# Performance work log

Measured on AMD Instinct MI355X. Metric: run time of the kernel, lower is better.

Reference implementation:

```python
import jax, jax.numpy as jnp
from jax import lax
import numpy as np

N_FFT = 256
HOP = 128
NUM_EXPERTS = 8
TOPK = 2
B = 128
L = 4096


def conv1d(x, w, b, pad):
    # x [N,C,T], w [O,I,K]
    y = lax.conv_general_dilated(x, w, (1,), [(pad, pad)],
                                 dimension_numbers=('NCH', 'OIH', 'NCH'))
    return y + b[None, :, None]


def maxpool1d(x, p):
    return lax.reduce_window(x, -jnp.inf, lax.max, (1, 1, p), (1, 1, p), 'VALID')


def se_block(x, w1, w2):
    # x [B,C,T]; squeeze-excitation with no-bias linears
    y = x.mean(-1)
    y = jax.nn.relu(y @ w1.T)
    y = jax.nn.sigmoid(y @ w2.T)
    return x * y[:, :, None]


def interp_linear(x, out_len):
    # F.interpolate(mode='linear', align_corners=False) on [B,C,T]
    Lin = x.shape[-1]
    scale = Lin / out_len
    coords = jnp.clip((jnp.arange(out_len, dtype=x.dtype) + 0.5) * scale - 0.5, 0.0, Lin - 1)
    lo = jnp.floor(coords).astype(jnp.int32)
    hi = jnp.minimum(lo + 1, Lin - 1)
    w = (coords - lo).astype(x.dtype)
    return x[..., lo] * (1.0 - w) + x[..., hi] * w


def lstm_scan(x, wih, whh, bih, bhh):
    # x [T,B,D] -> hidden seq [T,B,H]; torch gate order i,f,g,o
    H = whh.shape[1]
    def step(carry, xt):
        h, c = carry
        gates = xt @ wih.T + h @ whh.T + bih + bhh
        i, f, g, o = jnp.split(gates, 4, axis=-1)
        c = jax.nn.sigmoid(f) * c + jax.nn.sigmoid(i) * jnp.tanh(g)
        h = jax.nn.sigmoid(o) * jnp.tanh(c)
        return (h, c), h
    z = jnp.zeros((x.shape[1], H), x.dtype)
    _, hs = lax.scan(step, (z, z), x)
    return hs


def _forward(x_continuum, x_normalized,
             gate_w1, gate_b1, gate_w2, gate_b2,
             exp_w1, exp_b1, exp_w2, exp_b2,
             lw1, lb1, lw2, lb2, se2_w1, se2_w2, lw3, lb3, se3_w1, se3_w2,
             wih_f, whh_f, bih_f, bhh_f, wih_b, whh_b, bih_b, bhh_b,
             ffn_w1, ffn_b1, ffn_w2, ffn_b2):
    Bsz = x_continuum.shape[0]
    # --- STFT magnitude (center=True, reflect pad, periodic hann window) ---
    n = jnp.arange(N_FFT, dtype=x_continuum.dtype)
    win = 0.5 * (1.0 - jnp.cos(2.0 * jnp.pi * n / N_FFT))
    xp = jnp.pad(x_continuum, ((0, 0), (N_FFT // 2, N_FFT // 2)), mode='reflect')
    n_frames = 1 + (xp.shape[1] - N_FFT) // HOP  # 33
    idx = jnp.arange(n_frames)[:, None] * HOP + jnp.arange(N_FFT)[None, :]
    frames = xp[:, idx] * win                      # [B,T,N_FFT]
    mag = jnp.abs(jnp.fft.rfft(frames, axis=-1)).transpose(0, 2, 1)  # [B,129,T]
    mag = mag.astype(x_continuum.dtype)
    # --- gating: mean-pool over time, MLP, top-k, softmax over top-k ---
    pooled = mag.mean(-1)                          # [B,129]
    logits = jax.nn.relu(pooled @ gate_w1.T + gate_b1) @ gate_w2.T + gate_b2
    topv, topi = lax.top_k(logits, TOPK)
    gw = jax.nn.softmax(topv, axis=1)              # [B,K]
    # --- dense all-expert conv pyramids (matches original dense compute) ---
    def expert(w1, b1, w2, b2):
        h = jax.nn.relu(conv1d(mag, w1, b1, 2))
        return jax.nn.relu(conv1d(h, w2, b2, 1))
    eo = jax.vmap(expert)(exp_w1, exp_b1, exp_w2, exp_b2)  # [E,B,C,T]
    sel = eo[topi, jnp.arange(Bsz)[:, None]]               # [B,K,C,T]
    freq_feat = jnp.einsum('bk,bkct->bct', gw, sel)        # [B,256,33]
    # --- line attention branch ---
    h = jax.nn.relu(conv1d(x_normalized[:, None, :], lw1, lb1, 3))
    h = maxpool1d(h, 4)
    h = jax.nn.relu(conv1d(h, lw2, lb2, 2))
    h = se_block(h, se2_w1, se2_w2)
    h = maxpool1d(h, 4)
    h = jax.nn.relu(conv1d(h, lw3, lb3, 1))
    h = se_block(h, se3_w1, se3_w2)
    line_feat = maxpool1d(h, 4)                            # [B,256,64]
    # --- length alignment via linear interpolation ---
    t = min(freq_feat.shape[-1], line_feat.shape[-1])
    freq_feat = interp_linear(freq_feat, t)
    line_feat = interp_linear(line_feat, t)
    comb = jnp.concatenate([freq_feat, line_feat], axis=1).transpose(2, 0, 1)  # [T,B,512]
    # --- single-layer bidirectional LSTM, take last time step ---
    hf = lstm_scan(comb, wih_f, whh_f, bih_f, bhh_f)
    hb = lstm_scan(comb[::-1], wih_b, whh_b, bih_b, bhh_b)[::-1]
    last = jnp.concatenate([hf[-1], hb[-1]], axis=-1)      # [B,512]
    # --- prediction head (dropout inactive at inference) ---
    h = jax.nn.relu(last @ ffn_w1.T + ffn_b1)
    return h @ ffn_w2.T + ffn_b2                           # [B,1]


def setup_inputs() -> dict:
    key = jax.random.key(0)
    ks = jax.random.split(key, 40)
    def rn(k, shape, s=0.05):
        return jax.random.normal(k, shape, dtype=jnp.float32) * s
    d = {
        'x_continuum': jax.random.normal(ks[0], (B, L), jnp.float32),
        'x_normalized': jax.random.normal(ks[1], (B, L), jnp.float32),
        'gate_w1': rn(ks[2], (128, 129)), 'gate_b1': rn(ks[3], (128,)),
        'gate_w2': rn(ks[4], (NUM_EXPERTS, 128)), 'gate_b2': rn(ks[5], (NUM_EXPERTS,)),
        'exp_w1': rn(ks[6], (NUM_EXPERTS, 256, 129, 5)), 'exp_b1': rn(ks[7], (NUM_EXPERTS, 256)),
        'exp_w2': rn(ks[8], (NUM_EXPERTS, 256, 256, 3)), 'exp_b2': rn(ks[9], (NUM_EXPERTS, 256)),
        'lw1': rn(ks[10], (64, 1, 7)), 'lb1': rn(ks[11], (64,)),
        'lw2': rn(ks[12], (128, 64, 5)), 'lb2': rn(ks[13], (128,)),
        'se2_w1': rn(ks[14], (32, 128)), 'se2_w2': rn(ks[15], (128, 32)),
        'lw3': rn(ks[16], (256, 128, 3)), 'lb3': rn(ks[17], (256,)),
        'se3_w1': rn(ks[18], (64, 256)), 'se3_w2': rn(ks[19], (256, 64)),
        'wih_f': rn(ks[20], (1024, 512)), 'whh_f': rn(ks[21], (1024, 256)),
        'bih_f': rn(ks[22], (1024,)), 'bhh_f': rn(ks[23], (1024,)),
        'wih_b': rn(ks[24], (1024, 512)), 'whh_b': rn(ks[25], (1024, 256)),
        'bih_b': rn(ks[26], (1024,)), 'bhh_b': rn(ks[27], (1024,)),
        'ffn_w1': rn(ks[28], (256, 512)), 'ffn_b1': rn(ks[29], (256,)),
        'ffn_w2': rn(ks[30], (1, 256)), 'ffn_b2': rn(ks[31], (1,)),
    }
    return d


def reference(x_continuum, x_normalized,
              gate_w1, gate_b1, gate_w2, gate_b2,
              exp_w1, exp_b1, exp_w2, exp_b2,
              lw1, lb1, lw2, lb2, se2_w1, se2_w2, lw3, lb3, se3_w1, se3_w2,
              wih_f, whh_f, bih_f, bhh_f, wih_b, whh_b, bih_b, bhh_b,
              ffn_w1, ffn_b1, ffn_w2, ffn_b2):
    return _forward(x_continuum, x_normalized,
                    gate_w1, gate_b1, gate_w2, gate_b2,
                    exp_w1, exp_b1, exp_w2, exp_b2,
                    lw1, lb1, lw2, lb2, se2_w1, se2_w2, lw3, lb3, se3_w1, se3_w2,
                    wih_f, whh_f, bih_f, bhh_f, wih_b, whh_b, bih_b, bhh_b,
                    ffn_w1, ffn_b1, ffn_w2, ffn_b2)
```

## Files before the change

kernel.cpp:

```cpp
#include <hip/hip_runtime.h>
#include <math.h>

namespace {
constexpr int B = 128;
constexpr int L = 4096;
constexpr int NBIN = 129;
constexpr int NFR = 33;

constexpr size_t F_MAG    = 0;
constexpr size_t F_GW     = F_MAG + 544896;
constexpr size_t F_TOPI   = F_GW + 256;
constexpr size_t F_EH1    = F_TOPI + 256;
constexpr size_t F_SEL    = F_EH1 + 2162688;
constexpr size_t F_LINEF  = F_SEL + 2162688;
constexpr size_t F_COMB   = F_LINEF + 2097152;
constexpr size_t F_XPROJ  = F_COMB + 2162688;
constexpr size_t F_GATESB = F_XPROJ + 4325376;
constexpr size_t F_HF     = F_GATESB + 131072;
constexpr size_t F_HBLAST = F_HF + 32768;
constexpr size_t F_SESUM2 = F_HBLAST + 32768;
constexpr size_t F_SESC2  = F_SESUM2 + 16384;
constexpr size_t F_SESUM3 = F_SESC2 + 16384;
constexpr size_t F_SESC3  = F_SESUM3 + 32768;
constexpr size_t F_WHHB   = F_SESC3 + 32768;
constexpr size_t F_WKB    = F_WHHB + 131072;
constexpr size_t F_WKB3   = F_WKB + 20480;
constexpr size_t F_WIHF   = F_WKB3 + 49152;
constexpr size_t F_WIHB   = F_WIHF + 262144;
constexpr size_t F_BIGA   = F_WIHB + 262144;
constexpr size_t F_BIGB   = F_BIGA + 8388608;
constexpr size_t A_WKBE1  = F_XPROJ;
constexpr size_t A_WKBE2  = F_XPROJ + 720896;
constexpr size_t A_MAGT   = F_XPROJ + 1507328;
}

typedef __attribute__((ext_vector_type(8))) short bf16x8;
typedef __attribute__((ext_vector_type(4))) float f32x4;

__device__ __forceinline__ float sigm(float x) { return 1.0f / (1.0f + expf(-x)); }
__device__ __forceinline__ float fsigm(float x) { return 1.0f / (1.0f + __expf(-x)); }
__device__ __forceinline__ float ftanh(float x) { return 1.0f - 2.0f / (__expf(2.0f * x) + 1.0f); }

__device__ __forceinline__ unsigned int f2bf_rne(float f) {
    unsigned int u = __float_as_uint(f);
    return (u + 0x7FFFu + ((u >> 16) & 1u)) >> 16;
}
__device__ __forceinline__ float bflo(unsigned int u) { return __uint_as_float(u << 16); }
__device__ __forceinline__ float bfhi(unsigned int u) { return __uint_as_float(u & 0xFFFF0000u); }

__global__ __launch_bounds__(256) void stft_kernel(const float* __restrict__ x,
                                                   float* __restrict__ mag,
                                                   unsigned short* __restrict__ magT)
{
    int bf = blockIdx.x;
    int b = bf / NFR, f = bf % NFR;
    int tid = threadIdx.x;
    __shared__ float tbl[256];
    __shared__ float fx[256];
    tbl[tid] = cosf(6.28318530717958647692f * (float)tid / 256.0f);
    __syncthreads();
    {
        int j = f * 128 + tid - 128;
        if (j < 0) j = -j;
        else if (j >= L) j = 2 * L - 2 - j;
        float win = 0.5f * (1.0f - tbl[tid]);
        fx[tid] = x[(size_t)b * L + j] * win;
    }
    __syncthreads();
    if (tid < NBIN) {
        float re = 0.f, im = 0.f;
        int m = 0;
        for (int n = 0; n < 256; ++n) {
            float v = fx[n];
            re += v * tbl[m];
            im += v * tbl[(m + 192) & 255];
            m = (m + tid) & 255;
        }
        float val = sqrtf(re * re + im * im);
        mag[((size_t)b * NBIN + tid) * NFR + f] = val;
        magT[((size_t)b * NFR + f) * 136 + tid] = (unsigned short)f2bf_rne(val);
    } else if (tid < 136) {
        magT[((size_t)b * NFR + f) * 136 + tid] = 0;
    }
}

__global__ __launch_bounds__(128) void gate_kernel(const float* __restrict__ mag,
                                                   const float* __restrict__ w1,
                                                   const float* __restrict__ b1,
                                                   const float* __restrict__ w2,
                                                   const float* __restrict__ b2,
                                                   int* __restrict__ topi,
                                                   float* __restrict__ gw)
{
    int b = blockIdx.x, tid = threadIdx.x;
    __shared__ float pooled[NBIN];
    __shared__ float h1[128];
    __shared__ float lg[8];
    for (int k = tid; k < NBIN; k += 128) {
        const float* mp = mag + ((size_t)b * NBIN + k) * NFR;
        float s = 0.f;
        for (int f = 0; f < NFR; ++f) s += mp[f];
        pooled[k] = s * (1.0f / 33.0f);
    }
    __syncthreads();
    {
        float acc = b1[tid];
        const float* wr = w1 + tid * NBIN;
        for (int k = 0; k < NBIN; ++k) acc += pooled[k] * wr[k];
        h1[tid] = fmaxf(acc, 0.f);
    }
    __syncthreads();
    if (tid < 8) {
        float a = b2[tid];
        const float* w = w2 + tid * 128;
        for (int j = 0; j < 128; ++j) a += h1[j] * w[j];
        lg[tid] = a;
    }
    __syncthreads();
    if (tid == 0) {
        int i0 = 0; float v0 = lg[0];
        for (int e = 1; e < 8; ++e) if (lg[e] > v0) { v0 = lg[e]; i0 = e; }
        int i1 = -1; float v1 = -3.0e38f;
        for (int e = 0; e < 8; ++e) { if (e == i0) continue; if (lg[e] > v1) { v1 = lg[e]; i1 = e; } }
        float m = fmaxf(v0, v1);
        float e0 = expf(v0 - m), e1 = expf(v1 - m);
        float inv = 1.0f / (e0 + e1);
        topi[b * 2 + 0] = i0; topi[b * 2 + 1] = i1;
        gw[b * 2 + 0] = e0 * inv; gw[b * 2 + 1] = e1 * inv;
    }
}

__global__ __launch_bounds__(256) void prep_wkbE1_kernel(const float* __restrict__ W,
                                                         unsigned short* __restrict__ out)
{
    int idx = blockIdx.x * 256 + threadIdx.x;
    if (idx >= 8 * 256 * 704) return;
    int eo = idx / 704, K = idx % 704;
    int k = K / 136, ic = K - k * 136;
    float v = (k < 5 && ic < 129) ? W[((size_t)eo * 129 + ic) * 5 + k] : 0.f;
    out[idx] = (unsigned short)f2bf_rne(v);
}

__global__ __launch_bounds__(256) void prep_wkbE2_kernel(const float* __restrict__ W,
                                                         unsigned short* __restrict__ out)
{
    int idx = blockIdx.x * 256 + threadIdx.x;
    if (idx >= 8 * 256 * 768) return;
    int eo = idx / 768, K = idx % 768;
    int k = K >> 8, ic = K & 255;
    out[idx] = (unsigned short)f2bf_rne(W[((size_t)eo * 256 + ic) * 3 + k]);
}

__global__ __launch_bounds__(256) void expert_conv1_mfma(const unsigned short* __restrict__ magT,
                                                         const int* __restrict__ topi,
                                                         const unsigned short* __restrict__ wkbE1,
                                                         const float* __restrict__ Bb,
                                                         unsigned short* __restrict__ eh1T)
{
    int b = blockIdx.x, slot = blockIdx.y, ocq = blockIdx.z;
    int e = topi[b * 2 + slot];
    __shared__ __align__(16) unsigned short wl[64 * 704];
    __shared__ __align__(16) unsigned short inT[37 * 136];
    __shared__ float bias[64];
    int tid = threadIdx.x;
    for (int idx = tid; idx < 64 * 88; idx += 256) {
        int oc = idx / 88, ch = idx % 88;
        int swz = (ch & ~7) | ((ch & 7) ^ (oc & 7));
        *reinterpret_cast<uint4*>(&wl[oc * 704 + swz * 8]) =
            *reinterpret_cast<const uint4*>(&wkbE1[((size_t)(e * 256 + ocq * 64 + oc)) * 704 + ch * 8]);
    }
    for (int idx = tid; idx < 37 * 17; idx += 256) {
        int j = idx / 17, ch = idx % 17;
        int tp = j - 2;
        uint4 v = make_uint4(0u, 0u, 0u, 0u);
        if (tp >= 0 && tp < 33)
            v = *reinterpret_cast<const uint4*>(&magT[((size_t)b * NFR + tp) * 136 + ch * 8]);
        *reinterpret_cast<uint4*>(&inT[j * 136 + ch * 8]) = v;
    }
    if (tid < 64) bias[tid] = Bb[e * 256 + ocq * 64 + tid];
    __syncthreads();

    int lane = tid & 63, w = tid >> 6, l15 = lane & 15, g = lane >> 4;
    f32x4 acc[3];
#pragma unroll
    for (int n = 0; n < 3; ++n) acc[n] = (f32x4){0.f, 0.f, 0.f, 0.f};

    int row = w * 16 + l15;
    for (int ks = 0; ks < 22; ++ks) {
        int ch = ks * 4 + g;
        bf16x8 af = *reinterpret_cast<const bf16x8*>(
            &wl[row * 704 + (((ch & ~7) | ((ch & 7) ^ (row & 7)))) * 8]);
        int ce = ch > 84 ? 84 : ch;
        int k = ce / 17, icc = ce - k * 17;
#pragma unroll
        for (int n = 0; n < 3; ++n) {
            int t = n * 16 + l15;
            int j = t + k; if (j > 36) j = 36;
            bf16x8 bf = *reinterpret_cast<const bf16x8*>(&inT[j * 136 + icc * 8]);
            acc[n] = __builtin_amdgcn_mfma_f32_16x16x32_bf16(af, bf, acc[n], 0, 0, 0);
        }
    }
#pragma unroll
    for (int n = 0; n < 3; ++n) {
// ... 69 lines not shown
#pragma unroll
            for (int r = 0; r < 4; ++r) {
                int oc = ocq * 64 + w * 16 + g * 4 + r;
                float v = fmaxf(acc[n][r] + bias[w * 16 + g * 4 + r], 0.f);
                sel[(((size_t)b * 2 + slot) * 256 + oc) * NFR + t] = v;
            }
        }
    }
}

__global__ __launch_bounds__(256) void line1_kernel(const float* __restrict__ x,
                                                    const float* __restrict__ lw1,
                                                    const float* __restrict__ lb1,
                                                    unsigned short* __restrict__ p1T)
{
    int b = blockIdx.x;
    int P0 = blockIdx.y * 256;
    __shared__ float sx[1032];
    __shared__ float w[448];
    __shared__ float bb[64];
    __shared__ unsigned short sT[256 * 65];
    int tid = threadIdx.x;
    for (int i = tid; i < 448; i += 256) w[i] = lw1[i];
    for (int i = tid; i < 64; i += 256) bb[i] = lb1[i];
    int base = 4 * P0 - 3;
    for (int i = tid; i < 1032; i += 256) {
        int g = base + i;
        sx[i] = (g >= 0 && g < L) ? x[(size_t)b * L + g] : 0.f;
    }
    __syncthreads();
    int p = tid;
    for (int oc = 0; oc < 64; ++oc) {
        const float* wr = w + oc * 7;
        float best = -3.0e38f;
#pragma unroll
        for (int q = 0; q < 4; ++q) {
            const float* s = sx + 4 * p + q;
            float v = wr[0]*s[0] + wr[1]*s[1] + wr[2]*s[2] + wr[3]*s[3] + wr[4]*s[4] + wr[5]*s[5] + wr[6]*s[6];
            best = fmaxf(best, v);
        }
        float v = fmaxf(best + bb[oc], 0.f);
        sT[p * 65 + oc] = (unsigned short)f2bf_rne(v);
    }
    __syncthreads();
    unsigned int* outw = reinterpret_cast<unsigned int*>(p1T);
    for (int i2 = tid; i2 < 256 * 32; i2 += 256) {
        int row = i2 >> 5, dw = i2 & 31;
        unsigned int lo = sT[row * 65 + dw * 2];
        unsigned int hi = sT[row * 65 + dw * 2 + 1];
        outw[((size_t)b * 1024 + P0 + row) * 32 + dw] = lo | (hi << 16);
    }
}

__global__ __launch_bounds__(256) void prep_wkb_kernel(const float* __restrict__ W,
                                                       unsigned short* __restrict__ wkb)
{
    int idx = blockIdx.x * 256 + threadIdx.x;
    if (idx >= 128 * 320) return;
    int oc = idx / 320, K = idx % 320;
    int k = K >> 6, ic = K & 63;
    wkb[idx] = (unsigned short)f2bf_rne(W[oc * 320 + ic * 5 + k]);
}

__global__ __launch_bounds__(256) void line2_mfma_kernel(const unsigned short* __restrict__ p1T,
                                                         const unsigned short* __restrict__ wkb,
                                                         const float* __restrict__ lb2,
                                                         float* __restrict__ h2,
                                                         float* __restrict__ seSum2)
{
    int b = blockIdx.x;
    int t0 = blockIdx.y * 128;
    __shared__ __align__(16) unsigned short wl[128 * 320];
    __shared__ __align__(16) unsigned short inT[132 * 64];
    __shared__ float bias[128];
    int tid = threadIdx.x;

    for (int idx = tid; idx < 128 * 40; idx += 256) {
        int oc = idx / 40, ch = idx % 40;
        int swz = (ch & ~7) | ((ch & 7) ^ (oc & 7));
        *reinterpret_cast<uint4*>(&wl[oc * 320 + swz * 8]) =
            *reinterpret_cast<const uint4*>(&wkb[oc * 320 + ch * 8]);
    }
    for (int idx = tid; idx < 132 * 8; idx += 256) {
        int j = idx / 8, ch = idx % 8;
        int t = t0 - 2 + j;
        uint4 v = make_uint4(0u, 0u, 0u, 0u);
        if (t >= 0 && t < 1024)
            v = *reinterpret_cast<const uint4*>(&p1T[((size_t)b * 1024 + t) * 64 + ch * 8]);
        int swz = ch ^ (j & 7);
        *reinterpret_cast<uint4*>(&inT[j * 64 + swz * 8]) = v;
    }
    if (tid < 128) bias[tid] = lb2[tid];
    __syncthreads();

    int lane = tid & 63;
    int w = tid >> 6;
    int l15 = lane & 15, g = lane >> 4;

    f32x4 acc[8][2];
#pragma unroll
    for (int ot = 0; ot < 8; ++ot) {
        acc[ot][0] = (f32x4){0.f, 0.f, 0.f, 0.f};
        acc[ot][1] = (f32x4){0.f, 0.f, 0.f, 0.f};
    }

    for (int ks = 0; ks < 10; ++ks) {
        int k = ks >> 1;
        bf16x8 bf0, bf1;
        {
            int j = w * 32 + l15 + k;
            int ch = (ks & 1) * 4 + g;
            bf0 = *reinterpret_cast<const bf16x8*>(&inT[j * 64 + (ch ^ (j & 7)) * 8]);
            int j1 = j + 16;
            bf1 = *reinterpret_cast<const bf16x8*>(&inT[j1 * 64 + (ch ^ (j1 & 7)) * 8]);
        }
#pragma unroll
        for (int ot = 0; ot < 8; ++ot) {
            int row = ot * 16 + l15;
            int ch = ks * 4 + g;
            int swz = (ch & ~7) | ((ch & 7) ^ (row & 7));
            bf16x8 af = *reinterpret_cast<const bf16x8*>(&wl[row * 320 + swz * 8]);
            acc[ot][0] = __builtin_amdgcn_mfma_f32_16x16x32_bf16(af, bf0, acc[ot][0], 0, 0, 0);
            acc[ot][1] = __builtin_amdgcn_mfma_f32_16x16x32_bf16(af, bf1, acc[ot][1], 0, 0, 0);
        }
    }

    int tcol = t0 + w * 32 + l15;
#pragma unroll
    for (int ot = 0; ot < 8; ++ot) {
#pragma unroll
        for (int r = 0; r < 4; ++r) {
            int oc = ot * 16 + g * 4 + r;
            float bv = bias[oc];
            float v0 = fmaxf(acc[ot][0][r] + bv, 0.f);
            float v1 = fmaxf(acc[ot][1][r] + bv, 0.f);
            float* hp = h2 + ((size_t)b * 128 + oc) * 1024 + tcol;
            hp[0] = v0;
            hp[16] = v1;
            float s = v0 + v1;
            s += __shfl_xor(s, 1);
            s += __shfl_xor(s, 2);
            s += __shfl_xor(s, 4);
            s += __shfl_xor(s, 8);
            if (l15 == 0) atomicAdd(&seSum2[b * 128 + oc], s);
        }
    }
}

__global__ __launch_bounds__(128) void se2_kernel(const float* __restrict__ seSum2,
                                                  const float* __restrict__ w1,
                                                  const float* __restrict__ w2,
                                                  float* __restrict__ seScale2)
{
    int b = blockIdx.x, tid = threadIdx.x;
    __shared__ float y[128];
    __shared__ float z[32];
    y[tid] = seSum2[b * 128 + tid] * (1.0f / 1024.0f);
    __syncthreads();
    if (tid < 32) {
        float a = 0.f;
        const float* wr = w1 + tid * 128;
        for (int c = 0; c < 128; ++c) a += y[c] * wr[c];
        z[tid] = fmaxf(a, 0.f);
    }
    __syncthreads();
    {
        float a = 0.f;
        const float* wr = w2 + tid * 32;
        for (int j = 0; j < 32; ++j) a += z[j] * wr[j];
        seScale2[b * 128 + tid] = sigm(a);
    }
}

__global__ __launch_bounds__(256) void pool2t_kernel(const float* __restrict__ h2,
                                                     const float* __restrict__ seScale2,
                                                     unsigned short* __restrict__ p2T)
{
    int b = blockIdx.x, p = threadIdx.x;
    __shared__ unsigned short sT[256 * 129];
    for (int c = 0; c < 128; ++c) {
        float4 v = *reinterpret_cast<const float4*>(&h2[((size_t)b * 128 + c) * 1024 + 4 * p]);
        float m = fmaxf(fmaxf(v.x, v.y), fmaxf(v.z, v.w)) * seScale2[b * 128 + c];
        sT[p * 129 + c] = (unsigned short)f2bf_rne(m);
    }
    __syncthreads();
    unsigned int* out = reinterpret_cast<unsigned int*>(p2T);
    for (int idx = p; idx < 256 * 64; idx += 256) {
        int row = idx >> 6, dw = idx & 63;
        unsigned int lo = sT[row * 129 + dw * 2];
        unsigned int hi = sT[row * 129 + dw * 2 + 1];
        out[((size_t)b * 256 + row) * 64 + dw] = lo | (hi << 16);
    }
}

__global__ __launch_bounds__(256) void prep_wkb3_kernel(const float* __restrict__ W,
                                                        unsigned short* __restrict__ wkb3)
{
    int idx = blockIdx.x * 256 + threadIdx.x;
    if (idx >= 256 * 384) return;
    int oc = idx / 384, K = idx % 384;
    int k = K >> 7, ic = K & 127;
    wkb3[idx] = (unsigned short)f2bf_rne(W[oc * 384 + ic * 3 + k]);
}

__global__ __launch_bounds__(256) void line3_mfma_kernel(const unsigned short* __restrict__ p2T,
                                                         const unsigned short* __restrict__ wkb3,
                                                         const float* __restrict__ lb3,
                                                         float* __restrict__ h3,
                                                         float* __restrict__ seSum3)
{
    int b = blockIdx.x;
    int oc0 = blockIdx.y * 128;
    int t0 = blockIdx.z * 128;
    __shared__ __align__(16) unsigned short wl[128 * 384];
    __shared__ __align__(16) unsigned short inT[130 * 128];
    __shared__ float bias[128];
    int tid = threadIdx.x;

    for (int idx = tid; idx < 128 * 48; idx += 256) {
        int oc = idx / 48, ch = idx % 48;
        int swz = (ch & ~7) | ((ch & 7) ^ (oc & 7));
        *reinterpret_cast<uint4*>(&wl[oc * 384 + swz * 8]) =
            *reinterpret_cast<const uint4*>(&wkb3[(size_t)(oc0 + oc) * 384 + ch * 8]);
    }
    for (int idx = tid; idx < 130 * 16; idx += 256) {
        int j = idx / 16, ch = idx % 16;
        int t = t0 - 1 + j;
        uint4 v = make_uint4(0u, 0u, 0u, 0u);
        if (t >= 0 && t < 256)
            v = *reinterpret_cast<const uint4*>(&p2T[((size_t)b * 256 + t) * 128 + ch * 8]);
        int swz = ch ^ (j & 15);
        *reinterpret_cast<uint4*>(&inT[j * 128 + swz * 8]) = v;
    }
    if (tid < 128) bias[tid] = lb3[oc0 + tid];
    __syncthreads();

    int lane = tid & 63;
    int w = tid >> 6;
    int l15 = lane & 15, g = lane >> 4;

    f32x4 acc[8][2];
#pragma unroll
    for (int ot = 0; ot < 8; ++ot) {
        acc[ot][0] = (f32x4){0.f, 0.f, 0.f, 0.f};
        acc[ot][1] = (f32x4){0.f, 0.f, 0.f, 0.f};
    }

    for (int ks = 0; ks < 12; ++ks) {
        int k = ks >> 2;
        int ch = (ks & 3) * 4 + g;
        bf16x8 bf0, bf1;
        {
            int j = w * 32 + l15 + k;
            bf0 = *reinterpret_cast<const bf16x8*>(&inT[j * 128 + (ch ^ (j & 15)) * 8]);
            int j1 = j + 16;
            bf1 = *reinterpret_cast<const bf16x8*>(&inT[j1 * 128 + (ch ^ (j1 & 15)) * 8]);
        }
#pragma unroll
        for (int ot = 0; ot < 8; ++ot) {
            int row = ot * 16 + l15;
            int wch = ks * 4 + g;
            int swz = (wch & ~7) | ((wch & 7) ^ (row & 7));
            bf16x8 af = *reinterpret_cast<const bf16x8*>(&wl[row * 384 + swz * 8]);
            acc[ot][0] = __builtin_amdgcn_mfma_f32_16x16x32_bf16(af, bf0, acc[ot][0], 0, 0, 0);
            acc[ot][1] = __builtin_amdgcn_mfma_f32_16x16x32_bf16(af, bf1, acc[ot][1], 0, 0, 0);
        }
    }

    int tcol = t0 + w * 32 + l15;
#pragma unroll
    for (int ot = 0; ot < 8; ++ot) {
#pragma unroll
        for (int r = 0; r < 4; ++r) {
            int ocl = ot * 16 + g * 4 + r;
            int oc = oc0 + ocl;
            float bv = bias[ocl];
            float v0 = fmaxf(acc[ot][0][r] + bv, 0.f);
            float v1 = fmaxf(acc[ot][1][r] + bv, 0.f);
            float* hp = h3 + ((size_t)b * 256 + oc) * 256 + tcol;
            hp[0] = v0;
            hp[16] = v1;
            float s = v0 + v1;
            s += __shfl_xor(s, 1);
            s += __shfl_xor(s, 2);
            s += __shfl_xor(s, 4);
            s += __shfl_xor(s, 8);
            if (l15 == 0) atomicAdd(&seSum3[b * 256 + oc], s);
        }
    }
}

__global__ __launch_bounds__(256) void se3_kernel(const float* __restrict__ seSum3,
                                                  const float* __restrict__ w1,
                                                  const float* __restrict__ w2,
                                                  float* __restrict__ seScale3)
{
    int b = blockIdx.x, tid = threadIdx.x;
    __shared__ float y[256];
    __shared__ float z[64];
    y[tid] = seSum3[b * 256 + tid] * (1.0f / 256.0f);
    __syncthreads();
    if (tid < 64) {
        float a = 0.f;
        const float* wr = w1 + tid * 256;
        for (int c = 0; c < 256; ++c) a += y[c] * wr[c];
        z[tid] = fmaxf(a, 0.f);
    }
    __syncthreads();
    {
        float a = 0.f;
        const float* wr = w2 + tid * 64;
        for (int j = 0; j < 64; ++j) a += z[j] * wr[j];
        seScale3[b * 256 + tid] = sigm(a);
    }
}

__global__ __launch_bounds__(256) void pool3_kernel(const float* __restrict__ h3,
                                                    const float* __restrict__ seScale3,
                                                    float* __restrict__ lineFeat)
{
    const int total = 128 * 256 * 64;
    for (int idx = blockIdx.x * 256 + threadIdx.x; idx < total; idx += gridDim.x * 256) {
        int b = idx >> 14;
        int c = (idx >> 6) & 255;
        int p = idx & 63;
        const float* hp = h3 + (((size_t)b * 256 + c) * 256) + 4 * p;
        float v = fmaxf(fmaxf(hp[0], hp[1]), fmaxf(hp[2], hp[3]));
        lineFeat[idx] = v * seScale3[b * 256 + c];
    }
}

__global__ __launch_bounds__(256) void comb_kernel(const float* __restrict__ sel,
                                                   const float* __restrict__ gw,
                                                   const float* __restrict__ lineFeat,
                                                   unsigned short* __restrict__ combB)
{
    const int total = 33 * 128 * 512;
    for (int idx = blockIdx.x * 256 + threadIdx.x; idx < total; idx += gridDim.x * 256) {
        int c = idx & 511;
        int r = idx >> 9;
        int b = r & 127;
        int t = r >> 7;
        float v;
        if (c < 256) {
            float g0 = gw[b * 2 + 0], g1 = gw[b * 2 + 1];
            v = g0 * sel[(((size_t)b * 2 + 0) * 256 + c) * NFR + t]
              + g1 * sel[(((size_t)b * 2 + 1) * 256 + c) * NFR + t];
        } else {
            int cc = c - 256;
            float xc = ((float)t + 0.5f) * (64.0f / 33.0f) - 0.5f;
            xc = fminf(fmaxf(xc, 0.0f), 63.0f);
            int lo = (int)floorf(xc);
            int hi = lo + 1; if (hi > 63) hi = 63;
            float w = xc - (float)lo;
            const float* lp = lineFeat + ((size_t)b * 256 + cc) * 64;
            v = lp[lo] * (1.0f - w) + lp[hi] * w;
        }
        combB[idx] = (unsigned short)f2bf_rne(v);
    }
}

__global__ __launch_bounds__(256) void pack_bf16_kernel(const float* __restrict__ in,
                                                        unsigned short* __restrict__ out,
                                                        int n)
{
    int i = (blockIdx.x * 256 + threadIdx.x) * 4;
    if (i >= n) return;
    float4 v = *reinterpret_cast<const float4*>(in + i);
    uint2 w;
    w.x = f2bf_rne(v.x) | (f2bf_rne(v.y) << 16);
    w.y = f2bf_rne(v.z) | (f2bf_rne(v.w) << 16);
    *reinterpret_cast<uint2*>(out + i) = w;
}

__global__ __launch_bounds__(256) void gemm_mfma_kernel(const unsigned short* __restrict__ A,
                                                        const unsigned short* __restrict__ W,
                                                        const float* __restrict__ b1,
                                                        const float* __restrict__ b2,
                                                        float* __restrict__ out)
{
    int row0 = blockIdx.x * 128;
    int col0 = blockIdx.y * 128;
    __shared__ __align__(16) unsigned short As[128 * 64];
    __shared__ __align__(16) unsigned short Bs[128 * 64];
    __shared__ float bias[128];
    int tid = threadIdx.x;
    if (tid < 128) bias[tid] = b1[col0 + tid] + b2[col0 + tid];
    int lane = tid & 63, w = tid >> 6, l15 = lane & 15, g = lane >> 4;

    f32x4 acc[8][2];
#pragma unroll
    for (int ot = 0; ot < 8; ++ot) {
        acc[ot][0] = (f32x4){0.f, 0.f, 0.f, 0.f};
        acc[ot][1] = (f32x4){0.f, 0.f, 0.f, 0.f};
    }

    for (int kc = 0; kc < 8; ++kc) {
        __syncthreads();
        for (int idx = tid; idx < 1024; idx += 256) {
            int r = idx >> 3, ch = idx & 7;
            int swz = ch ^ (r & 7);
            *reinterpret_cast<uint4*>(&As[r * 64 + swz * 8]) =
                *reinterpret_cast<const uint4*>(&A[(size_t)(row0 + r) * 512 + kc * 64 + ch * 8]);
            *reinterpret_cast<uint4*>(&Bs[r * 64 + swz * 8]) =
                *reinterpret_cast<const uint4*>(&W[(size_t)(col0 + r) * 512 + kc * 64 + ch * 8]);
        }
        __syncthreads();
#pragma unroll
        for (int ks = 0; ks < 2; ++ks) {
            int ch = ks * 4 + g;
            int j = w * 32 + l15;
            bf16x8 bf0 = *reinterpret_cast<const bf16x8*>(&As[j * 64 + (ch ^ (j & 7)) * 8]);
            int j1 = j + 16;
            bf16x8 bf1 = *reinterpret_cast<const bf16x8*>(&As[j1 * 64 + (ch ^ (j1 & 7)) * 8]);
#pragma unroll
            for (int ot = 0; ot < 8; ++ot) {
                int row = ot * 16 + l15;
                bf16x8 af = *reinterpret_cast<const bf16x8*>(&Bs[row * 64 + (ch ^ (row & 7)) * 8]);
                acc[ot][0] = __builtin_amdgcn_mfma_f32_16x16x32_bf16(af, bf0, acc[ot][0], 0, 0, 0);
                acc[ot][1] = __builtin_amdgcn_mfma_f32_16x16x32_bf16(af, bf1, acc[ot][1], 0, 0, 0);
            }
        }
    }

    int rbase = row0 + w * 32 + l15;
#pragma unroll
    for (int ot = 0; ot < 8; ++ot) {
#pragma unroll
        for (int r = 0; r < 4; ++r) {
            int ocl = ot * 16 + g * 4 + r;
            float bv = bias[ocl];
            out[(size_t)rbase * 1024 + col0 + ocl] = acc[ot][0][r] + bv;
            out[(size_t)(rbase + 16) * 1024 + col0 + ocl] = acc[ot][1][r] + bv;
        }
    }
}

__global__ __launch_bounds__(256) void prep_whh4_kernel(const float* __restrict__ W,
                                                        uint4* __restrict__ whh4)
{
    int idx = blockIdx.x * 256 + threadIdx.x;
    int k8 = idx >> 10, j = idx & 1023;
    const float* src = W + (size_t)j * 256 + k8 * 8;
    float4 v0 = *reinterpret_cast<const float4*>(src);
    float4 v1 = *reinterpret_cast<const float4*>(src + 4);
    uint4 w;
    w.x = f2bf_rne(v0.x) | (f2bf_rne(v0.y) << 16);
    w.y = f2bf_rne(v0.z) | (f2bf_rne(v0.w) << 16);
    w.z = f2bf_rne(v1.x) | (f2bf_rne(v1.y) << 16);
    w.w = f2bf_rne(v1.z) | (f2bf_rne(v1.w) << 16);
    whh4[(size_t)k8 * 1024 + j] = w;
}

__global__ __launch_bounds__(1024) void lstm_fused_kernel(const float* __restrict__ xproj,
                                                          const uint4* __restrict__ whh4,
                                                          float* __restrict__ hfinal)
{
    int b = blockIdx.x;
    int j = threadIdx.x;
    __shared__ __align__(16) float h[256];
    __shared__ float cc[256];
    __shared__ float g[1024];
    if (j < 256) { h[j] = 0.f; cc[j] = 0.f; }
    __syncthreads();
    const uint4* wp = whh4 + j;
    for (int t = 0; t < 33; ++t) {
        float a0 = xproj[(size_t)t * 131072 + (size_t)b * 1024 + j];
        float a1 = 0.f;
#pragma unroll 8
        for (int k8 = 0; k8 < 32; ++k8) {
            uint4 w = wp[k8 << 10];
            float4 h0 = *reinterpret_cast<const float4*>(&h[k8 * 8]);
            float4 h1 = *reinterpret_cast<const float4*>(&h[k8 * 8 + 4]);
            a0 += bflo(w.x) * h0.x + bfhi(w.x) * h0.y + bflo(w.y) * h0.z + bfhi(w.y) * h0.w;
            a1 += bflo(w.z) * h1.x + bfhi(w.z) * h1.y + bflo(w.w) * h1.z + bfhi(w.w) * h1.w;
        }
        g[j] = a0 + a1;
        __syncthreads();
        if (j < 256) {
            float gi = g[j], gf = g[256 + j], gz = g[512 + j], go = g[768 + j];
            float c = fsigm(gf) * cc[j] + fsigm(gi) * ftanh(gz);
            cc[j] = c;
            h[j] = fsigm(go) * ftanh(c);
        }
        __syncthreads();
    }
    if (j < 256) hfinal[b * 256 + j] = h[j];
}

__global__ __launch_bounds__(256) void lstm_bwd_tail_kernel(const float* __restrict__ gatesB,
                                                            float* __restrict__ hbLast)
{
    int b = blockIdx.x, u = threadIdx.x;
    const float* g = gatesB + (size_t)b * 1024;
    float ai = g[u], ag = g[512 + u], ao = g[768 + u];
    float c = sigm(ai) * tanhf(ag);
    hbLast[b * 256 + u] = sigm(ao) * tanhf(c);
}

__global__ __launch_bounds__(256) void ffn_kernel(const float* __restrict__ hf,
                                                  const float* __restrict__ hb,
                                                  const float* __restrict__ w1,
                                                  const float* __restrict__ b1,
                                                  const float* __restrict__ w2,
                                                  const float* __restrict__ b2,
                                                  float* __restrict__ out)
{
    int b = blockIdx.x, tid = threadIdx.x;
    __shared__ float last[512];
    __shared__ float red[256];
    last[tid] = hf[b * 256 + tid];
    last[256 + tid] = hb[b * 256 + tid];
    __syncthreads();
    float a = b1[tid];
    const float* wr = w1 + (size_t)tid * 512;
    for (int k = 0; k < 512; ++k) a += last[k] * wr[k];
    red[tid] = fmaxf(a, 0.f) * w2[tid];
    __syncthreads();
    for (int s = 128; s > 0; s >>= 1) {
        if (tid < s) red[tid] += red[tid + s];
        __syncthreads();
    }
    if (tid == 0) out[b] = red[0] + b2[0];
}

extern "C" void kernel_launch(void* const* d_in, const int* in_sizes, int n_in,
                              void* d_out, int out_size, void* d_ws, size_t ws_size,
                              hipStream_t stream)
{
    (void)in_sizes; (void)n_in; (void)out_size; (void)ws_size;
    const float* x_cont = (const float*)d_in[0];
    const float* x_norm = (const float*)d_in[1];
    const float* gate_w1 = (const float*)d_in[2];
    const float* gate_b1 = (const float*)d_in[3];
    const float* gate_w2 = (const float*)d_in[4];
    const float* gate_b2 = (const float*)d_in[5];
    const float* exp_w1 = (const float*)d_in[6];
    const float* exp_b1 = (const float*)d_in[7];
    const float* exp_w2 = (const float*)d_in[8];
    const float* exp_b2 = (const float*)d_in[9];
    const float* lw1 = (const float*)d_in[10];
    const float* lb1 = (const float*)d_in[11];
    const float* lw2 = (const float*)d_in[12];
    const float* lb2 = (const float*)d_in[13];
    const float* se2_w1 = (const float*)d_in[14];
    const float* se2_w2 = (const float*)d_in[15];
    const float* lw3 = (const float*)d_in[16];
    const float* lb3 = (const float*)d_in[17];
    const float* se3_w1 = (const float*)d_in[18];
    const float* se3_w2 = (const float*)d_in[19];
    const float* wih_f = (const float*)d_in[20];
    const float* whh_f = (const float*)d_in[21];
    const float* bih_f = (const float*)d_in[22];
    const float* bhh_f = (const float*)d_in[23];
    const float* wih_b = (const float*)d_in[24];
    const float* whh_b = (const float*)d_in[25];
    const float* bih_b = (const float*)d_in[26];
    const float* bhh_b = (const float*)d_in[27];
    const float* ffn_w1 = (const float*)d_in[28];
    const float* ffn_b1 = (const float*)d_in[29];
    const float* ffn_w2 = (const float*)d_in[30];
    const float* ffn_b2 = (const float*)d_in[31];

    float* ws = (float*)d_ws;
    float* mag     = ws + F_MAG;
    float* gw      = ws + F_GW;
    int*   topi    = (int*)(ws + F_TOPI);
    unsigned short* eh1T = (unsigned short*)(ws + F_EH1);
    float* sel     = ws + F_SEL;
    float* lineFeat= ws + F_LINEF;
    unsigned short* combB = (unsigned short*)(ws + F_COMB);
    float* xproj   = ws + F_XPROJ;
    float* gatesB  = ws + F_GATESB;
    float* hfF     = ws + F_HF;
    float* hbLast  = ws + F_HBLAST;
    float* seSum2  = ws + F_SESUM2;
    float* seSc2   = ws + F_SESC2;
    float* seSum3  = ws + F_SESUM3;
    float* seSc3   = ws + F_SESC3;
    uint4* whh4    = (uint4*)(ws + F_WHHB);
    unsigned short* wkb  = (unsigned short*)(ws + F_WKB);
    unsigned short* wkb3 = (unsigned short*)(ws + F_WKB3);
    unsigned short* wihFb = (unsigned short*)(ws + F_WIHF);
    unsigned short* wihBb = (unsigned short*)(ws + F_WIHB);
    unsigned short* wkbE1 = (unsigned short*)(ws + A_WKBE1);
    unsigned short* wkbE2 = (unsigned short*)(ws + A_WKBE2);
    unsigned short* magT  = (unsigned short*)(ws + A_MAGT);
    unsigned short* p1T = (unsigned short*)(ws + F_BIGA);
    float* h2      = ws + F_BIGB;
    unsigned short* p2T = (unsigned short*)(ws + F_BIGA);
    float* h3      = ws + F_BIGB;

    hipMemsetAsync(seSum2, 0, 16384 * sizeof(float), stream);
    hipMemsetAsync(seSum3, 0, 32768 * sizeof(float), stream);

    prep_wkbE1_kernel<<<5632, 256, 0, stream>>>(exp_w1, wkbE1);
    prep_wkbE2_kernel<<<6144, 256, 0, stream>>>(exp_w2, wkbE2);

    stft_kernel<<<B * NFR, 256, 0, stream>>>(x_cont, mag, magT);
    gate_kernel<<<B, 128, 0, stream>>>(mag, gate_w1, gate_b1, gate_w2, gate_b2, topi, gw);
    expert_conv1_mfma<<<dim3(B, 2, 4), 256, 0, stream>>>(magT, topi, wkbE1, exp_b1, eh1T);
    expert_conv2_mfma<<<dim3(B, 2, 4), 256, 0, stream>>>(eh1T, topi, wkbE2, exp_b2, sel);

    prep_wkb_kernel<<<160, 256, 0, stream>>>(lw2, wkb);
    line1_kernel<<<dim3(B, 4), 256, 0, stream>>>(x_norm, lw1, lb1, p1T);
    line2_mfma_kernel<<<dim3(B, 8), 256, 0, stream>>>(p1T, wkb, lb2, h2, seSum2);
    se2_kernel<<<B, 128, 0, stream>>>(seSum2, se2_w1, se2_w2, seSc2);
    pool2t_kernel<<<B, 256, 0, stream>>>(h2, seSc2, p2T);
    prep_wkb3_kernel<<<384, 256, 0, stream>>>(lw3, wkb3);
    line3_mfma_kernel<<<dim3(B, 2, 2), 256, 0, stream>>>(p2T, wkb3, lb3, h3, seSum3);
    se3_kernel<<<B, 256, 0, stream>>>(seSum3, se3_w1, se3_w2, seSc3);
    pool3_kernel<<<2048, 256, 0, stream>>>(h3, seSc3, lineFeat);

    comb_kernel<<<2048, 256, 0, stream>>>(sel, gw, lineFeat, combB);

    pack_bf16_kernel<<<512, 256, 0, stream>>>(wih_f, wihFb, 1024 * 512);
    pack_bf16_kernel<<<512, 256, 0, stream>>>(wih_b, wihBb, 1024 * 512);

    gemm_mfma_kernel<<<dim3(33, 8), 256, 0, stream>>>(combB, wihFb, bih_f, bhh_f, xproj);
    gemm_mfma_kernel<<<dim3(1, 8), 256, 0, stream>>>(combB + (size_t)4096 * 512, wihBb, bih_b, bhh_b, gatesB);
    lstm_bwd_tail_kernel<<<B, 256, 0, stream>>>(gatesB, hbLast);

    prep_whh4_kernel<<<128, 256, 0, stream>>>(whh_f, whh4);
    lstm_fused_kernel<<<B, 1024, 0, stream>>>(xproj, whh4, hfF);

    ffn_kernel<<<B, 256, 0, stream>>>(hfF, hbLast, ffn_w1, ffn_b1, ffn_w2, ffn_b2, (float*)d_out);
}
```

Measured before the change: 591.7 us.

## Merge weight-prep kernels, fuse SE into pooling, store conv activations as bf16

All weight-packing kernels and the two memsets become one prep_all kernel that dispatches on block index. The SE-scale computations are folded into the pool2t and pool3 kernels, and the LSTM backward tail moves into the FFN kernel, which removes several launches. The line2 and line3 conv outputs h2 and h3 are now stored as bf16 rather than fp32, halving that intermediate traffic at some cost in precision. pool3 now runs one block per batch instead of a grid-stride loop over 2048 blocks, so it has less parallelism.

```diff
diff --git a/kernel.cpp b/kernel.cpp
--- a/kernel.cpp
+++ b/kernel.cpp
@@ -32,6 +32,16 @@
 constexpr size_t A_WKBE1  = F_XPROJ;
 constexpr size_t A_WKBE2  = F_XPROJ + 720896;
 constexpr size_t A_MAGT   = F_XPROJ + 1507328;
+
+constexpr int PB_E1   = 5632;
+constexpr int PB_E2   = PB_E1 + 6144;
+constexpr int PB_WKB  = PB_E2 + 160;
+constexpr int PB_WKB3 = PB_WKB + 384;
+constexpr int PB_WF   = PB_WKB3 + 512;
+constexpr int PB_WB   = PB_WF + 512;
+constexpr int PB_WHH  = PB_WB + 128;
+constexpr int PB_Z2   = PB_WHH + 64;
+constexpr int PB_Z3   = PB_Z2 + 128;
 }
 
 typedef __attribute__((ext_vector_type(8))) short bf16x8;
@@ -47,6 +57,79 @@
 }
 __device__ __forceinline__ float bflo(unsigned int u) { return __uint_as_float(u << 16); }
 __device__ __forceinline__ float bfhi(unsigned int u) { return __uint_as_float(u & 0xFFFF0000u); }
+__device__ __forceinline__ float bf2f(unsigned short s) { return __uint_as_float(((unsigned int)s) << 16); }
+
+__global__ __launch_bounds__(256) void prep_all_kernel(const float* __restrict__ exp_w1,
+                                                       const float* __restrict__ exp_w2,
+                                                       const float* __restrict__ lw2,
+                                                       const float* __restrict__ lw3,
+                                                       const float* __restrict__ wih_f,
+                                                       const float* __restrict__ wih_b,
+                                                       const float* __restrict__ whh_f,
+                                                       unsigned short* __restrict__ wkbE1,
+                                                       unsigned short* __restrict__ wkbE2,
+                                                       unsigned short* __restrict__ wkb,
+                                                       unsigned short* __restrict__ wkb3,
+                                                       unsigned short* __restrict__ wihFb,
+                                                       unsigned short* __restrict__ wihBb,
+                                                       uint4* __restrict__ whh4,
+                                                       float* __restrict__ seSum2,
+                                                       float* __restrict__ seSum3)
+{
+    int bid = blockIdx.x, tid = threadIdx.x;
+    if (bid < PB_E1) {
+        int idx = bid * 256 + tid;
+        int eo = idx / 704, K = idx % 704;
+        int k = K / 136, ic = K - k * 136;
+        float v = (k < 5 && ic < 129) ? exp_w1[((size_t)eo * 129 + ic) * 5 + k] : 0.f;
+        wkbE1[idx] = (unsigned short)f2bf_rne(v);
+    } else if (bid < PB_E2) {
+        int idx = (bid - PB_E1) * 256 + tid;
+        int eo = idx / 768, K = idx % 768;
+        int k = K >> 8, ic = K & 255;
+        wkbE2[idx] = (unsigned short)f2bf_rne(exp_w2[((size_t)eo * 256 + ic) * 3 + k]);
+    } else if (bid < PB_WKB) {
+        int idx = (bid - PB_E2) * 256 + tid;
+        int oc = idx / 320, K = idx % 320;
+        int k = K >> 6, ic = K & 63;
+        wkb[idx] = (unsigned short)f2bf_rne(lw2[oc * 320 + ic * 5 + k]);
+    } else if (bid < PB_WKB3) {
+        int idx = (bid - PB_WKB) * 256 + tid;
+        int oc = idx / 384, K = idx % 384;
+        int k = K >> 7, ic = K & 127;
+        wkb3[idx] = (unsigned short)f2bf_rne(lw3[oc * 384 + ic * 3 + k]);
+    } else if (bid < PB_WF) {
+        int i = ((bid - PB_WKB3) * 256 + tid) * 4;
+        float4 v = *reinterpret_cast<const float4*>(wih_f + i);
+        uint2 w;
+        w.x = f2bf_rne(v.x) | (f2bf_rne(v.y) << 16);
+        w.y = f2bf_rne(v.z) | (f2bf_rne(v.w) << 16);
+        *reinterpret_cast<uint2*>(wihFb + i) = w;
+    } else if (bid < PB_WB) {
+        int i = ((bid - PB_WF) * 256 + tid) * 4;
+        float4 v = *reinterpret_cast<const float4*>(wih_b + i);
+        uint2 w;
+        w.x = f2bf_rne(v.x) | (f2bf_rne(v.y) << 16);
+        w.y = f2bf_rne(v.z) | (f2bf_rne(v.w) << 16);
+        *reinterpret_cast<uint2*>(wihBb + i) = w;
+    } else if (bid < PB_WHH) {
+        int idx = (bid - PB_WB) * 256 + tid;
+        int k8 = idx >> 10, j = idx & 1023;
+        const float* src = whh_f + (size_t)j * 256 + k8 * 8;
+        float4 v0 = *reinterpret_cast<const float4*>(src);
+        float4 v1 = *reinterpret_cast<const float4*>(src + 4);
+        uint4 w;
+        w.x = f2bf_rne(v0.x) | (f2bf_rne(v0.y) << 16);
+        w.y = f2bf_rne(v0.z) | (f2bf_rne(v0.w) << 16);
+        w.z = f2bf_rne(v1.x) | (f2bf_rne(v1.y) << 16);
+        w.w = f2bf_rne(v1.z) | (f2bf_rne(v1.w) << 16);
+        whh4[(size_t)k8 * 1024 + j] = w;
+    } else if (bid < PB_Z2) {
+        seSum2[(bid - PB_WHH) * 256 + tid] = 0.f;
+    } else {
+        seSum3[(bid - PB_Z2) * 256 + tid] = 0.f;
+    }
+}
 
 __global__ __launch_bounds__(256) void stft_kernel(const float* __restrict__ x,
                                                    float* __restrict__ mag,
@@ -128,27 +211,6 @@
         topi[b * 2 + 0] = i0; topi[b * 2 + 1] = i1;
         gw[b * 2 + 0] = e0 * inv; gw[b * 2 + 1] = e1 * inv;
     }
-}
-
-__global__ __launch_bounds__(256) void prep_wkbE1_kernel(const float* __restrict__ W,
-                                                         unsigned short* __restrict__ out)
-{
-    int idx = blockIdx.x * 256 + threadIdx.x;
-    if (idx >= 8 * 256 * 704) return;
-    int eo = idx / 704, K = idx % 704;
-    int k = K / 136, ic = K - k * 136;
-    float v = (k < 5 && ic < 129) ? W[((size_t)eo * 129 + ic) * 5 + k] : 0.f;
-    out[idx] = (unsigned short)f2bf_rne(v);
-}
-
-__global__ __launch_bounds__(256) void prep_wkbE2_kernel(const float* __restrict__ W,
-                                                         unsigned short* __restrict__ out)
-{
-    int idx = blockIdx.x * 256 + threadIdx.x;
-    if (idx >= 8 * 256 * 768) return;
-    int eo = idx / 768, K = idx % 768;
-    int k = K >> 8, ic = K & 255;
-    out[idx] = (unsigned short)f2bf_rne(W[((size_t)eo * 256 + ic) * 3 + k]);
 }
 
 __global__ __launch_bounds__(256) void expert_conv1_mfma(const unsigned short* __restrict__ magT,
@@ -324,20 +386,10 @@
     }
 }
 
-__global__ __launch_bounds__(256) void prep_wkb_kernel(const float* __restrict__ W,
-                                                       unsigned short* __restrict__ wkb)
-{
-    int idx = blockIdx.x * 256 + threadIdx.x;
-    if (idx >= 128 * 320) return;
-    int oc = idx / 320, K = idx % 320;
-    int k = K >> 6, ic = K & 63;
-    wkb[idx] = (unsigned short)f2bf_rne(W[oc * 320 + ic * 5 + k]);
-}
-
 __global__ __launch_bounds__(256) void line2_mfma_kernel(const unsigned short* __restrict__ p1T,
                                                          const unsigned short* __restrict__ wkb,
                                                          const float* __restrict__ lb2,
-                                                         float* __restrict__ h2,
+                                                         unsigned short* __restrict__ h2b,
                                                          float* __restrict__ seSum2)
 {
     int b = blockIdx.x;
@@ -406,9 +458,9 @@
             float bv = bias[oc];
             float v0 = fmaxf(acc[ot][0][r] + bv, 0.f);
             float v1 = fmaxf(acc[ot][1][r] + bv, 0.f);
-            float* hp = h2 + ((size_t)b * 128 + oc) * 1024 + tcol;
-            hp[0] = v0;
-            hp[16] = v1;
+            unsigned short* hp = h2b + ((size_t)b * 128 + oc) * 1024 + tcol;
+            hp[0] = (unsigned short)f2bf_rne(v0);
+            hp[16] = (unsigned short)f2bf_rne(v1);
             float s = v0 + v1;
             s += __shfl_xor(s, 1);
             s += __shfl_xor(s, 2);
@@ -419,40 +471,36 @@
     }
 }
 
-__global__ __launch_bounds__(128) void se2_kernel(const float* __restrict__ seSum2,
-                                                  const float* __restrict__ w1,
-                                                  const float* __restrict__ w2,
-                                                  float* __restrict__ seScale2)
-{
-    int b = blockIdx.x, tid = threadIdx.x;
+__global__ __launch_bounds__(256) void pool2t_kernel(const unsigned short* __restrict__ h2b,
+                                                     const float* __restrict__ seSum2,
+                                                     const float* __restrict__ w1,
+                                                     const float* __restrict__ w2,
+                                                     unsigned short* __restrict__ p2T)
+{
+    int b = blockIdx.x, p = threadIdx.x;
     __shared__ float y[128];
     __shared__ float z[32];
-    y[tid] = seSum2[b * 128 + tid] * (1.0f / 1024.0f);
-    __syncthreads();
-    if (tid < 32) {
+    __shared__ float scale[128];
+    __shared__ unsigned short sT[256 * 129];
+    if (p < 128) y[p] = seSum2[b * 128 + p] * (1.0f / 1024.0f);
+    __syncthreads();
+    if (p < 32) {
         float a = 0.f;
-        const float* wr = w1 + tid * 128;
+        const float* wr = w1 + p * 128;
         for (int c = 0; c < 128; ++c) a += y[c] * wr[c];
-        z[tid] = fmaxf(a, 0.f);
-    }
-    __syncthreads();
-    {
+        z[p] = fmaxf(a, 0.f);
+    }
+    __syncthreads();
+    if (p < 128) {
         float a = 0.f;
-        const float* wr = w2 + tid * 32;
+        const float* wr = w2 + p * 32;
         for (int j = 0; j < 32; ++j) a += z[j] * wr[j];
-        seScale2[b * 128 + tid] = sigm(a);
-    }
-}
-
-__global__ __launch_bounds__(256) void pool2t_kernel(const float* __restrict__ h2,
-                                                     const float* __restrict__ seScale2,
-                                                     unsigned short* __restrict__ p2T)
-{
-    int b = blockIdx.x, p = threadIdx.x;
-    __shared__ unsigned short sT[256 * 129];
+        scale[p] = sigm(a);
+    }
+    __syncthreads();
     for (int c = 0; c < 128; ++c) {
-        float4 v = *reinterpret_cast<const float4*>(&h2[((size_t)b * 128 + c) * 1024 + 4 * p]);
-        float m = fmaxf(fmaxf(v.x, v.y), fmaxf(v.z, v.w)) * seScale2[b * 128 + c];
+        uint2 v = *reinterpret_cast<const uint2*>(&h2b[((size_t)b * 128 + c) * 1024 + 4 * p]);
+        float m = fmaxf(fmaxf(bflo(v.x), bfhi(v.x)), fmaxf(bflo(v.y), bfhi(v.y))) * scale[c];
         sT[p * 129 + c] = (unsigned short)f2bf_rne(m);
     }
     __syncthreads();
@@ -465,20 +513,10 @@
     }
 }
 
-__global__ __launch_bounds__(256) void prep_wkb3_kernel(const float* __restrict__ W,
-                                                        unsigned short* __restrict__ wkb3)
-{
-    int idx = blockIdx.x * 256 + threadIdx.x;
-    if (idx >= 256 * 384) return;
-    int oc = idx / 384, K = idx % 384;
-    int k = K >> 7, ic = K & 127;
-    wkb3[idx] = (unsigned short)f2bf_rne(W[oc * 384 + ic * 3 + k]);
-}
-
 __global__ __launch_bounds__(256) void line3_mfma_kernel(const unsigned short* __restrict__ p2T,
                                                          const unsigned short* __restrict__ wkb3,
                                                          const float* __restrict__ lb3,
-                                                         float* __restrict__ h3,
+                                                         unsigned short* __restrict__ h3b,
                                                          float* __restrict__ seSum3)
 {
     int b = blockIdx.x;
@@ -549,9 +587,9 @@
             float bv = bias[ocl];
             float v0 = fmaxf(acc[ot][0][r] + bv, 0.f);
             float v1 = fmaxf(acc[ot][1][r] + bv, 0.f);
-            float* hp = h3 + ((size_t)b * 256 + oc) * 256 + tcol;
-            hp[0] = v0;
-            hp[16] = v1;
+            unsigned short* hp = h3b + ((size_t)b * 256 + oc) * 256 + tcol;
+            hp[0] = (unsigned short)f2bf_rne(v0);
+            hp[16] = (unsigned short)f2bf_rne(v1);
             float s = v0 + v1;
             s += __shfl_xor(s, 1);
             s += __shfl_xor(s, 2);
@@ -562,14 +600,16 @@
     }
 }
 
-__global__ __launch_bounds__(256) void se3_kernel(const float* __restrict__ seSum3,
-                                                  const float* __restrict__ w1,
-                                                  const float* __restrict__ w2,
-                                                  float* __restrict__ seScale3)
+__global__ __launch_bounds__(256) void pool3_kernel(const unsigned short* __restrict__ h3b,
+                                                    const float* __restrict__ seSum3,
+                                                    const float* __restrict__ w1,
+                                                    const float* __restrict__ w2,
+                                                    float* __restrict__ lineFeat)
 {
     int b = blockIdx.x, tid = threadIdx.x;
     __shared__ float y[256];
     __shared__ float z[64];
+    __shared__ float scale[256];
     y[tid] = seSum3[b * 256 + tid] * (1.0f / 256.0f);
     __syncthreads();
     if (tid < 64) {
@@ -583,22 +623,14 @@
         float a = 0.f;
         const float* wr = w2 + tid * 64;
         for (int j = 0; j < 64; ++j) a += z[j] * wr[j];
-        seScale3[b * 256 + tid] = sigm(a);
-    }
-}
-
-__global__ __launch_bounds__(256) void pool3_kernel(const float* __restrict__ h3,
-                                                    const float* __restrict__ seScale3,
-                                                    float* __restrict__ lineFeat)
-{
-    const int total = 128 * 256 * 64;
-    for (int idx = blockIdx.x * 256 + threadIdx.x; idx < total; idx += gridDim.x * 256) {
-        int b = idx >> 14;
-        int c = (idx >> 6) & 255;
-        int p = idx & 63;
-        const float* hp = h3 + (((size_t)b * 256 + c) * 256) + 4 * p;
-        float v = fmaxf(fmaxf(hp[0], hp[1]), fmaxf(hp[2], hp[3]));
-        lineFeat[idx] = v * seScale3[b * 256 + c];
+        scale[tid] = sigm(a);
+    }
+    __syncthreads();
+    for (int idx = tid; idx < 256 * 64; idx += 256) {
+        int c = idx >> 6, p = idx & 63;
+        uint2 v = *reinterpret_cast<const uint2*>(&h3b[(((size_t)b * 256 + c) * 256) + 4 * p]);
+        float m = fmaxf(fmaxf(bflo(v.x), bfhi(v.x)), fmaxf(bflo(v.y), bfhi(v.y)));
+        lineFeat[((size_t)b * 256 + c) * 64 + p] = m * scale[c];
     }
 }
 
@@ -632,19 +664,6 @@
     }
 }
 
-__global__ __launch_bounds__(256) void pack_bf16_kernel(const float* __restrict__ in,
-                                                        unsigned short* __restrict__ out,
-                                                        int n)
-{
-    int i = (blockIdx.x * 256 + threadIdx.x) * 4;
-    if (i >= n) return;
-    float4 v = *reinterpret_cast<const float4*>(in + i);
-    uint2 w;
-    w.x = f2bf_rne(v.x) | (f2bf_rne(v.y) << 16);
-    w.y = f2bf_rne(v.z) | (f2bf_rne(v.w) << 16);
-    *reinterpret_cast<uint2*>(out + i) = w;
-}
-
 __global__ __launch_bounds__(256) void gemm_mfma_kernel(const unsigned short* __restrict__ A,
                                                         const unsigned short* __restrict__ W,
                                                         const float* __restrict__ b1,
@@ -706,22 +725,6 @@
             out[(size_t)(rbase + 16) * 1024 + col0 + ocl] = acc[ot][1][r] + bv;
         }
     }
-}
-
-__global__ __launch_bounds__(256) void prep_whh4_kernel(const float* __restrict__ W,
-                                                        uint4* __restrict__ whh4)
-{
-    int idx = blockIdx.x * 256 + threadIdx.x;
-    int k8 = idx >> 10, j = idx & 1023;
-    const float* src = W + (size_t)j * 256 + k8 * 8;
-    float4 v0 = *reinterpret_cast<const float4*>(src);
-    float4 v1 = *reinterpret_cast<const float4*>(src + 4);
-    uint4 w;
-    w.x = f2bf_rne(v0.x) | (f2bf_rne(v0.y) << 16);
-    w.y = f2bf_rne(v0.z) | (f2bf_rne(v0.w) << 16);
-    w.z = f2bf_rne(v1.x) | (f2bf_rne(v1.y) << 16);
-    w.w = f2bf_rne(v1.z) | (f2bf_rne(v1.w) << 16);
-    whh4[(size_t)k8 * 1024 + j] = w;
 }
 
 __global__ __launch_bounds__(1024) void lstm_fused_kernel(const float* __restrict__ xproj,
@@ -760,18 +763,8 @@
     if (j < 256) hfinal[b * 256 + j] = h[j];
 }
 
-__global__ __launch_bounds__(256) void lstm_bwd_tail_kernel(const float* __restrict__ gatesB,
-                                                            float* __restrict__ hbLast)
-{
-    int b = blockIdx.x, u = threadIdx.x;
-    const float* g = gatesB + (size_t)b * 1024;
-    float ai = g[u], ag = g[512 + u], ao = g[768 + u];
-    float c = sigm(ai) * tanhf(ag);
-    hbLast[b * 256 + u] = sigm(ao) * tanhf(c);
-}
-
 __global__ __launch_bounds__(256) void ffn_kernel(const float* __restrict__ hf,
-                                                  const float* __restrict__ hb,
+                                                  const float* __restrict__ gatesB,
                                                   const float* __restrict__ w1,
                                                   const float* __restrict__ b1,
                                                   const float* __restrict__ w2,
@@ -782,7 +775,12 @@
     __shared__ float last[512];
     __shared__ float red[256];
     last[tid] = hf[b * 256 + tid];
-    last[256 + tid] = hb[b * 256 + tid];
+    {
+        const float* g = gatesB + (size_t)b * 1024;
+        float ai = g[tid], ag = g[512 + tid], ao = g[768 + tid];
+        float c = sigm(ai) * tanhf(ag);
+        last[256 + tid] = sigm(ao) * tanhf(c);
+    }
     __syncthreads();
     float a = b1[tid];
     const float* wr = w1 + (size_t)tid * 512;
@@ -845,11 +843,8 @@
     float* xproj   = ws + F_XPROJ;
     float* gatesB  = ws + F_GATESB;
     float* hfF     = ws + F_HF;
-    float* hbLast  = ws + F_HBLAST;
     float* seSum2  = ws + F_SESUM2;
-    float* seSc2   = ws + F_SESC2;
     float* seSum3  = ws + F_SESUM3;
-    float* seSc3   = ws + F_SESC3;
     uint4* whh4    = (uint4*)(ws + F_WHHB);
     unsigned short* wkb  = (unsigned short*)(ws + F_WKB);
     unsigned short* wkb3 = (unsigned short*)(ws + F_WKB3);
@@ -859,42 +854,31 @@
     unsigned short* wkbE2 = (unsigned short*)(ws + A_WKBE2);
     unsigned short* magT  = (unsigned short*)(ws + A_MAGT);
     unsigned short* p1T = (unsigned short*)(ws + F_BIGA);
-    float* h2      = ws + F_BIGB;
+    unsigned short* h2b = (unsigned short*)(ws + F_BIGB);
     unsigned short* p2T = (unsigned short*)(ws + F_BIGA);
-    float* h3      = ws + F_BIGB;
-
-    hipMemsetAsync(seSum2, 0, 16384 * sizeof(float), stream);
-    hipMemsetAsync(seSum3, 0, 32768 * sizeof(float), stream);
-
-    prep_wkbE1_kernel<<<5632, 256, 0, stream>>>(exp_w1, wkbE1);
-    prep_wkbE2_kernel<<<6144, 256, 0, stream>>>(exp_w2, wkbE2);
+    unsigned short* h3b = (unsigned short*)(ws + F_BIGB);
+
+    prep_all_kernel<<<PB_Z3, 256, 0, stream>>>(exp_w1, exp_w2, lw2, lw3, wih_f, wih_b, whh_f,
+                                               wkbE1, wkbE2, wkb, wkb3, wihFb, wihBb, whh4,
+                                               seSum2, seSum3);
 
     stft_kernel<<<B * NFR, 256, 0, stream>>>(x_cont, mag, magT);
     gate_kernel<<<B, 128, 0, stream>>>(mag, gate_w1, gate_b1, gate_w2, gate_b2, topi, gw);
     expert_conv1_mfma<<<dim3(B, 2, 4), 256, 0, stream>>>(magT, topi, wkbE1, exp_b1, eh1T);
     expert_conv2_mfma<<<dim3(B, 2, 4), 256, 0, stream>>>(eh1T, topi, wkbE2, exp_b2, sel);
 
-    prep_wkb_kernel<<<160, 256, 0, stream>>>(lw2, wkb);
     line1_kernel<<<dim3(B, 4), 256, 0, stream>>>(x_norm, lw1, lb1, p1T);
-    line2_mfma_kernel<<<dim3(B, 8), 256, 0, stream>>>(p1T, wkb, lb2, h2, seSum2);
-    se2_kernel<<<B, 128, 0, stream>>>(seSum2, se2_w1, se2_w2, seSc2);
-    pool2t_kernel<<<B, 256, 0, stream>>>(h2, seSc2, p2T);
-    prep_wkb3_kernel<<<384, 256, 0, stream>>>(lw3, wkb3);
-    line3_mfma_kernel<<<dim3(B, 2, 2), 256, 0, stream>>>(p2T, wkb3, lb3, h3, seSum3);
-    se3_kernel<<<B, 256, 0, stream>>>(seSum3, se3_w1, se3_w2, seSc3);
-    pool3_kernel<<<2048, 256, 0, stream>>>(h3, seSc3, lineFeat);
+    line2_mfma_kernel<<<dim3(B, 8), 256, 0, stream>>>(p1T, wkb, lb2, h2b, seSum2);
+    pool2t_kernel<<<B, 256, 0, stream>>>(h2b, seSum2, se2_w1, se2_w2, p2T);
+    line3_mfma_kernel<<<dim3(B, 2, 2), 256, 0, stream>>>(p2T, wkb3, lb3, h3b, seSum3);
+    pool3_kernel<<<B, 256, 0, stream>>>(h3b, seSum3, se3_w1, se3_w2, lineFeat);
 
     comb_kernel<<<2048, 256, 0, stream>>>(sel, gw, lineFeat, combB);
-
-    pack_bf16_kernel<<<512, 256, 0, stream>>>(wih_f, wihFb, 1024 * 512);
-    pack_bf16_kernel<<<512, 256, 0, stream>>>(wih_b, wihBb, 1024 * 512);
 
     gemm_mfma_kernel<<<dim3(33, 8), 256, 0, stream>>>(combB, wihFb, bih_f, bhh_f, xproj);
     gemm_mfma_kernel<<<dim3(1, 8), 256, 0, stream>>>(combB + (size_t)4096 * 512, wihBb, bih_b, bhh_b, gatesB);
-    lstm_bwd_tail_kernel<<<B, 256, 0, stream>>>(gatesB, hbLast);
-
-    prep_whh4_kernel<<<128, 256, 0, stream>>>(whh_f, whh4);
+
     lstm_fused_kernel<<<B, 1024, 0, stream>>>(xproj, whh4, hfF);
 
-    ffn_kernel<<<B, 256, 0, stream>>>(hfF, hbLast, ffn_w1, ffn_b1, ffn_w2, ffn_b2, (float*)d_out);
-}
+    ffn_kernel<<<B, 256, 0, stream>>>(hfF, gatesB, ffn_w1, ffn_b1, ffn_w2, ffn_b2, (float*)d_out);
+}
```

After: 562.4 us. 1.05x faster.
